# Performance work log

Hardware: AMD Instinct MI355X
Metric: run time of the kernel (lower is better)

The kernel has to match this reference:

```python
import jax, jax.numpy as jnp
import numpy as np

N = 50000
E = 800000
D_IN = 256
D_OUT = 256
EPS = 1.0 + 1e-06


def setup_inputs() -> dict:
    key = jax.random.key(0)
    ks = jax.random.split(key, 10)
    x = jax.random.normal(ks[0], (N, D_IN), dtype=jnp.float32)
    lower_indices = jax.random.randint(ks[1], (2, E), 0, N, dtype=jnp.int64)
    lower_values = jax.random.uniform(ks[2], (E,), dtype=jnp.float32)
    upper_indices = jax.random.randint(ks[3], (2, E), 0, N, dtype=jnp.int64)
    upper_values = jax.random.uniform(ks[4], (E,), dtype=jnp.float32)
    s = 1.0 / np.sqrt(D_IN)
    W_lower = jax.random.uniform(ks[5], (D_IN, D_OUT), jnp.float32, -s, s)
    att_lower = jax.random.uniform(ks[6], (2 * D_OUT,), jnp.float32, -s, s)
    W_upper = jax.random.uniform(ks[7], (D_IN, D_OUT), jnp.float32, -s, s)
    att_upper = jax.random.uniform(ks[8], (2 * D_OUT,), jnp.float32, -s, s)
    W_lin = jax.random.uniform(ks[9], (D_IN, D_OUT), jnp.float32, -s, s)
    return {"x": x, "lower_indices": lower_indices, "lower_values": lower_values,
            "upper_indices": upper_indices, "upper_values": upper_values,
            "W_lower": W_lower, "att_lower": att_lower,
            "W_upper": W_upper, "att_upper": att_upper, "W_lin": W_lin}


def can_conv(x, indices, values, W, att_weight):
    # x: [N, d_in]; indices: [2, E] (row=target i, col=source j); values: [E]
    n = x.shape[0]
    xm = x @ W                                    # [N, d_out]
    tgt, src = indices[0], indices[1]
    d = xm.shape[1]
    # attention: elu( [x_i ; x_j] . att_weight ) computed without concat
    score = jax.nn.elu(xm @ att_weight[:d])[tgt] + jax.nn.elu(0.0) * 0.0  # placeholder
    score = jax.nn.elu((xm @ att_weight[:d])[tgt] + (xm @ att_weight[d:])[src])  # [E]
    v = score * values                            # attention * neighborhood values
    # sparse row-wise softmax (per target index)
    m = jax.ops.segment_max(v, tgt, num_segments=n)
    e = jnp.exp(v - m[tgt])
    s = jax.ops.segment_sum(e, tgt, num_segments=n)
    a = e / s[tgt]                                # [E]
    # spmm: out[i] = sum_j a_ij * xm[j]
    return jax.ops.segment_sum(a[:, None] * xm[src], tgt, num_segments=n)


def reference(x, lower_indices, lower_values, upper_indices, upper_values,
              W_lower, att_lower, W_upper, att_upper, W_lin):
    lower_x = can_conv(x, lower_indices, lower_values, W_lower, att_lower)
    upper_x = can_conv(x, upper_indices, upper_values, W_upper, att_upper)
    w_x = (x @ W_lin) * EPS
    return jax.nn.relu(lower_x + upper_x + w_x)
```

## Files before the change

kernel.cpp:

```cpp
#include <hip/hip_runtime.h>
#include <hip/hip_bf16.h>


constexpr int N_NODES = 50000;
constexpr int N_EDGES = 800000;
constexpr int D = 256;
constexpr float EPSV = 1.0f + 1e-06f;

typedef __attribute__((ext_vector_type(8))) short short8;
typedef __attribute__((ext_vector_type(4))) float f32x4;

__device__ __forceinline__ unsigned short f2bf(float f) {
    unsigned int b = __float_as_uint(f);
    unsigned int r = (b + 0x7FFFu + ((b >> 16) & 1u)) >> 16;
    return (unsigned short)r;
}
__device__ __forceinline__ float bf2f(unsigned short u) {
    return __uint_as_float(((unsigned int)u) << 16);
}

__global__ __launch_bounds__(256) void cvt_x_kernel(
    const float4* __restrict__ x, ushort4* __restrict__ xb, int n4)
{
    int i = blockIdx.x * 256 + threadIdx.x;
    if (i >= n4) return;
    float4 v = x[i];
    ushort4 o;
    o.x = f2bf(v.x); o.y = f2bf(v.y); o.z = f2bf(v.z); o.w = f2bf(v.w);
    xb[i] = o;
}

__global__ __launch_bounds__(256) void cvt_w_kernel(
    const float* __restrict__ W0, const float* __restrict__ W1,
    const float* __restrict__ W2, unsigned short* __restrict__ wbT)
{
    int z = blockIdx.y;
    const float* W = (z == 0) ? W0 : (z == 1) ? W1 : W2;
    int n = blockIdx.x;
    int k = threadIdx.x;
    wbT[(size_t)z * 65536 + (size_t)n * 256 + k] = f2bf(W[(size_t)k * 256 + n]);
}

__global__ __launch_bounds__(256) void gemm_mfma_kernel(
    const unsigned short* __restrict__ xb, const unsigned short* __restrict__ wbT,
    unsigned short* __restrict__ xml, unsigned short* __restrict__ xmu,
    float* __restrict__ out, int M)
{
    const int wz = blockIdx.z;
    const int tid = threadIdx.x;
    const int w = tid >> 6, lane = tid & 63;
    const int r16 = lane & 15, g = lane >> 4;
    const int m0 = blockIdx.x * 128 + w * 32;
    const int n0 = blockIdx.y * 64;
    const unsigned short* wb = wbT + (size_t)wz * 65536;

    const int ar0 = min(m0 + r16, M - 1);
    const int ar1 = min(m0 + 16 + r16, M - 1);
    const unsigned short* pa0 = xb + (size_t)ar0 * 256 + 8 * g;
    const unsigned short* pa1 = xb + (size_t)ar1 * 256 + 8 * g;
    const unsigned short* pb  = wb + (size_t)(n0 + r16) * 256 + 8 * g;

    f32x4 acc[2][4];
    #pragma unroll
    for (int mf = 0; mf < 2; ++mf)
        #pragma unroll
        for (int nf = 0; nf < 4; ++nf)
            acc[mf][nf] = (f32x4){0.f, 0.f, 0.f, 0.f};

    #pragma unroll
    for (int kt = 0; kt < 256; kt += 32) {
        short8 a0 = *reinterpret_cast<const short8*>(pa0 + kt);
        short8 a1 = *reinterpret_cast<const short8*>(pa1 + kt);
        #pragma unroll
        for (int nf = 0; nf < 4; ++nf) {
            short8 bf = *reinterpret_cast<const short8*>(pb + (size_t)nf * 16 * 256 + kt);
            acc[0][nf] = __builtin_amdgcn_mfma_f32_16x16x32_bf16(a0, bf, acc[0][nf], 0, 0, 0);
            acc[1][nf] = __builtin_amdgcn_mfma_f32_16x16x32_bf16(a1, bf, acc[1][nf], 0, 0, 0);
        }
    }

    if (wz < 2) {
        unsigned short* dst = wz ? xmu : xml;
        #pragma unroll
        for (int mf = 0; mf < 2; ++mf)
            #pragma unroll
            for (int r = 0; r < 4; ++r) {
                int row = m0 + mf * 16 + g * 4 + r;
                if (row < M) {
                    #pragma unroll
                    for (int nf = 0; nf < 4; ++nf)
                        dst[(size_t)row * 256 + n0 + nf * 16 + r16] = f2bf(acc[mf][nf][r]);
                }
            }
    } else {
        #pragma unroll
        for (int mf = 0; mf < 2; ++mf)
            #pragma unroll
            for (int r = 0; r < 4; ++r) {
                int row = m0 + mf * 16 + g * 4 + r;
                if (row < M) {
                    #pragma unroll
                    for (int nf = 0; nf < 4; ++nf)
                        out[(size_t)row * 256 + n0 + nf * 16 + r16] = acc[mf][nf][r] * EPSV;
                }
            }
    }
}

__global__ __launch_bounds__(256) void att_kernel(
    const unsigned short* __restrict__ xm, const float* __restrict__ att,
    float* __restrict__ a, float* __restrict__ b, int n)
{
    int node = (int)((blockIdx.x * 256 + threadIdx.x) >> 6);
    int lane = threadIdx.x & 63;
    if (node >= n) return;
    ushort4 uv = *reinterpret_cast<const ushort4*>(xm + (size_t)node * 256 + lane * 4);
    float x0 = bf2f(uv.x), x1 = bf2f(uv.y), x2 = bf2f(uv.z), x3 = bf2f(uv.w);
    int o = lane * 4;
    float sa = x0 * att[o] + x1 * att[o + 1] + x2 * att[o + 2] + x3 * att[o + 3];
    float sb = x0 * att[D + o] + x1 * att[D + o + 1] + x2 * att[D + o + 2] + x3 * att[D + o + 3];
    #pragma unroll
    for (int off = 32; off; off >>= 1) {
        sa += __shfl_down(sa, off);
        sb += __shfl_down(sb, off);
    }
    if (lane == 0) { a[node] = sa; b[node] = sb; }
}

__global__ __launch_bounds__(256) void hist_kernel(
    const int* __restrict__ il, const int* __restrict__ iu,
    int* __restrict__ cl, int* __restrict__ cu)
{
    int e = blockIdx.x * 256 + threadIdx.x;
    if (e >= N_EDGES) return;
    atomicAdd(&cl[il[e]], 1);
    atomicAdd(&cu[iu[e]], 1);
}

__global__ __launch_bounds__(1024) void scan_local_kernel(
    const int* __restrict__ cnt0, int* __restrict__ ro0,
    const int* __restrict__ cnt1, int* __restrict__ ro1,
    int* __restrict__ bsum, int n)
{
    int c = blockIdx.y;
    const int* cnt = c ? cnt1 : cnt0;
    int* ro = c ? ro1 : ro0;
    __shared__ int sm[1024];
    int tid = threadIdx.x;
    int i = blockIdx.x * 1024 + tid;
    int v = (i < n) ? cnt[i] : 0;
    sm[tid] = v;
    __syncthreads();
    #pragma unroll
    for (int off = 1; off < 1024; off <<= 1) {
        int t = (tid >= off) ? sm[tid - off] : 0;
        __syncthreads();
        sm[tid] += t;
        __syncthreads();
    }
    if (i < n) ro[i] = sm[tid] - v;
    if (tid == 1023) bsum[c * 64 + blockIdx.x] = sm[1023];
}

__global__ __launch_bounds__(128) void scan_bsum_kernel(int* __restrict__ bsum, int nb)
{
    int c = threadIdx.x >> 6, lane = threadIdx.x & 63;
    int v = (lane < nb) ? bsum[c * 64 + lane] : 0;
    int orig = v;
    #pragma unroll
    for (int off = 1; off < 64; off <<= 1) {
        int t = __shfl_up(v, off);
        if (lane >= off) v += t;
    }
    if (lane < nb) bsum[c * 64 + lane] = v - orig;
}

__global__ __launch_bounds__(256) void scan_apply_kernel(
    int* __restrict__ ro0, int* __restrict__ ro1,
    const int* __restrict__ bsum, int n)
{
    int c = blockIdx.y;
    int* ro = c ? ro1 : ro0;
    int i = blockIdx.x * 256 + threadIdx.x;
    if (i < n) ro[i] += bsum[c * 64 + (i >> 10)];
    if (i == 0) ro[n] = N_EDGES;
}

__global__ __launch_bounds__(256) void scatter_kernel(
    const int* __restrict__ il, const float* __restrict__ vl,
    const int* __restrict__ rol, int* __restrict__ curl, int2* __restrict__ egl,
    const int* __restrict__ iu, const float* __restrict__ vu,
    const int* __restrict__ rou, int* __restrict__ curu, int2* __restrict__ egu)
{
    int e = blockIdx.x * 256 + threadIdx.x;
    if (e >= N_EDGES) return;
    int tl = il[e];
    int pl = rol[tl] + atomicAdd(&curl[tl], 1);
    int2 p; p.x = il[N_EDGES + e]; p.y = __float_as_int(vl[e]);
    egl[pl] = p;
    int tu = iu[e];
    int pu = rou[tu] + atomicAdd(&curu[tu], 1);
    int2 q; q.x = iu[N_EDGES + e]; q.y = __float_as_int(vu[e]);
    egu[pu] = q;
}

__device__ __forceinline__ float wave_sum(float v) {
    #pragma unroll
    for (int off = 32; off; off >>= 1) v += __shfl_xor(v, off);
    return v;
}

__device__ __forceinline__ void conv_accum(
    int node, int lane,
    const int* __restrict__ ro, const int2* __restrict__ eg,
    const float* __restrict__ a, const float* __restrict__ b,
    const unsigned short* __restrict__ xm, float4& acc)
{
    int rs = ro[node], re = ro[node + 1];
    int deg = re - rs;
    if (deg <= 0) return;
    float ai = a[node];
    if (deg <= 64) {
        float evl = 0.f; int srcl = 0;
        if (lane < deg) {
            int2 p = eg[rs + lane];
            srcl = p.x;
            float xv = ai + b[srcl];
            float sc = (xv > 0.f) ? xv : (expf(xv) - 1.f);
            evl = expf(sc * __int_as_float(p.y));
        }
        float invs = 1.f / wave_sum(evl);
        for (int t = 0; t < deg; ++t) {
            float w = __shfl(evl, t) * invs;
            int si = __shfl(srcl, t);
            ushort4 uv = *reinterpret_cast<const ushort4*>(xm + (size_t)si * 256 + lane * 4);
            acc.x += w * bf2f(uv.x); acc.y += w * bf2f(uv.y);
            acc.z += w * bf2f(uv.z); acc.w += w * bf2f(uv.w);
        }
    } else {
        float s = 0.f;
        for (int c = rs; c < re; c += 64) {
            int m = min(64, re - c);
            float evl = 0.f;
            if (lane < m) {
                int2 p = eg[c + lane];
                float xv = ai + b[p.x];
                float sc = (xv > 0.f) ? xv : (expf(xv) - 1.f);
                evl = expf(sc * __int_as_float(p.y));
            }
            s += wave_sum(evl);
        }
        float invs = 1.f / s;
        for (int c = rs; c < re; c += 64) {
            int m = min(64, re - c);
            float evl = 0.f; int srcl = 0;
            if (lane < m) {
                int2 p = eg[c + lane];
                srcl = p.x;
                float xv = ai + b[srcl];
                float sc = (xv > 0.f) ? xv : (expf(xv) - 1.f);
                evl = expf(sc * __int_as_float(p.y));
            }
            for (int t = 0; t < m; ++t) {
                float w = __shfl(evl, t) * invs;
                int si = __shfl(srcl, t);
                ushort4 uv = *reinterpret_cast<const ushort4*>(xm + (size_t)si * 256 + lane * 4);
                acc.x += w * bf2f(uv.x); acc.y += w * bf2f(uv.y);
                acc.z += w * bf2f(uv.z); acc.w += w * bf2f(uv.w);
            }
        }
    }
}

__global__ __launch_bounds__(256) void gather_kernel(
    const int* __restrict__ rol, const int2* __restrict__ egl,
    const float* __restrict__ al, const float* __restrict__ bl,
    const unsigned short* __restrict__ xml,
    const int* __restrict__ rou, const int2* __restrict__ egu,
    const float* __restrict__ au, const float* __restrict__ bu,
    const unsigned short* __restrict__ xmu,
    float4* __restrict__ out)
{
    int node = (int)((blockIdx.x * 256 + threadIdx.x) >> 6);
    int lane = threadIdx.x & 63;
    if (node >= N_NODES) return;
    float4 acc = make_float4(0.f, 0.f, 0.f, 0.f);
    conv_accum(node, lane, rol, egl, al, bl, xml, acc);
    conv_accum(node, lane, rou, egu, au, bu, xmu, acc);
    float4 xw = out[(size_t)node * 64 + lane];
    acc.x = fmaxf(acc.x + xw.x, 0.f);
    acc.y = fmaxf(acc.y + xw.y, 0.f);
    acc.z = fmaxf(acc.z + xw.z, 0.f);
    acc.w = fmaxf(acc.w + xw.w, 0.f);
    out[(size_t)node * 64 + lane] = acc;
}

extern "C" void kernel_launch(void* const* d_in, const int* in_sizes, int n_in,
                              void* d_out, int out_size, void* d_ws, size_t ws_size,
                              hipStream_t stream)
{
    (void)in_sizes; (void)n_in; (void)out_size; (void)ws_size;
    const float* x        = (const float*)d_in[0];
    const int*   low_idx  = (const int*)  d_in[1];
    const float* low_vals = (const float*)d_in[2];
    const int*   up_idx   = (const int*)  d_in[3];
    const float* up_vals  = (const float*)d_in[4];
    const float* W_lower  = (const float*)d_in[5];
    const float* att_low  = (const float*)d_in[6];
    const float* W_upper  = (const float*)d_in[7];
    const float* att_up   = (const float*)d_in[8];
    const float* W_lin    = (const float*)d_in[9];
    float* out = (float*)d_out;

    char* ws = (char*)d_ws;
    size_t off = 0;
    auto alloc = [&](size_t bytes) {
        void* p = ws + off;
        off += (bytes + 255) & ~(size_t)255;
        return p;
    };
    unsigned short* xb     = (unsigned short*)alloc((size_t)N_NODES * D * 2);
    unsigned short* wbT    = (unsigned short*)alloc((size_t)3 * 256 * 256 * 2);
    unsigned short* xm_low = (unsigned short*)alloc((size_t)N_NODES * D * 2);
    unsigned short* xm_up  = (unsigned short*)alloc((size_t)N_NODES * D * 2);
    float* a_low  = (float*)alloc(N_NODES * 4);
    float* b_low  = (float*)alloc(N_NODES * 4);
    float* a_up   = (float*)alloc(N_NODES * 4);
    float* b_up   = (float*)alloc(N_NODES * 4);
    int* zero_blk = (int*)alloc(4 * N_NODES * 4);
    int* cnt_low = zero_blk;
    int* cnt_up  = zero_blk + N_NODES;
    int* cur_low = zero_blk + 2 * N_NODES;
    int* cur_up  = zero_blk + 3 * N_NODES;
    int* ro_low  = (int*)alloc((N_NODES + 1) * 4);
    int* ro_up   = (int*)alloc((N_NODES + 1) * 4);
    int* bsum    = (int*)alloc(2 * 64 * 4);
    int2* eg_low = (int2*)alloc((size_t)N_EDGES * 8);
    int2* eg_up  = (int2*)alloc((size_t)N_EDGES * 8);

    hipMemsetAsync(zero_blk, 0, 4 * N_NODES * 4, stream);

    int n4 = N_NODES * D / 4;
    cvt_x_kernel<<<(n4 + 255) / 256, 256, 0, stream>>>(
        (const float4*)x, (ushort4*)xb, n4);
    dim3 wgrid(256, 3);
    cvt_w_kernel<<<wgrid, 256, 0, stream>>>(W_lower, W_upper, W_lin, wbT);

    dim3 ggrid((N_NODES + 127) / 128, D / 64, 3);
    gemm_mfma_kernel<<<ggrid, 256, 0, stream>>>(xb, wbT, xm_low, xm_up, out, N_NODES);

    int ablocks = (N_NODES + 3) / 4;
    att_kernel<<<ablocks, 256, 0, stream>>>(xm_low, att_low, a_low, b_low, N_NODES);
    att_kernel<<<ablocks, 256, 0, stream>>>(xm_up,  att_up,  a_up,  b_up,  N_NODES);

    int eblocks = (N_EDGES + 255) / 256;
    hist_kernel<<<eblocks, 256, 0, stream>>>(low_idx, up_idx, cnt_low, cnt_up);
    dim3 sgrid((N_NODES + 1023) / 1024, 2);
    scan_local_kernel<<<sgrid, 1024, 0, stream>>>(cnt_low, ro_low, cnt_up, ro_up,
                                                  bsum, N_NODES);
    scan_bsum_kernel<<<1, 128, 0, stream>>>(bsum, (N_NODES + 1023) / 1024);
    dim3 agrid((N_NODES + 255) / 256, 2);
    scan_apply_kernel<<<agrid, 256, 0, stream>>>(ro_low, ro_up, bsum, N_NODES);
    scatter_kernel<<<eblocks, 256, 0, stream>>>(
        low_idx, low_vals, ro_low, cur_low, eg_low,
        up_idx,  up_vals,  ro_up,  cur_up,  eg_up);

    int gblocks = (N_NODES + 3) / 4;
    gather_kernel<<<gblocks, 256, 0, stream>>>(
        ro_low, eg_low, a_low, b_low, xm_low,
        ro_up,  eg_up,  a_up,  b_up,  xm_up,
        (float4*)out);
}
```

Measured before the change: 538.3 us.

## Fuse attention projections into GEMM, record edge ranks in histogram, unroll gather

The GEMM kernel now computes all three weight products per 32-row tile in one block and reduces the attention dot products from the fp32 accumulators through shared memory, removing the two separate att_kernel passes over xm. The histogram kernel stores each edge's atomic rank so the scatter kernel no longer needs a second round of atomics or the cur arrays. The gather inner loop is unrolled by two to keep two row loads in flight. The costs are higher register pressure from 24 accumulator tiles per wave, and extra rank buffers that must be written and read back.

After: 483.5 us. 10.2% less time.

```diff
diff --git a/kernel.cpp b/kernel.cpp
--- a/kernel.cpp
+++ b/kernel.cpp
@@ -41,100 +41,128 @@
     wbT[(size_t)z * 65536 + (size_t)n * 256 + k] = f2bf(W[(size_t)k * 256 + n]);
 }
 
-__global__ __launch_bounds__(256) void gemm_mfma_kernel(
+__global__ __launch_bounds__(256) void gemm_fused_kernel(
     const unsigned short* __restrict__ xb, const unsigned short* __restrict__ wbT,
+    const float* __restrict__ att_l, const float* __restrict__ att_u,
     unsigned short* __restrict__ xml, unsigned short* __restrict__ xmu,
-    float* __restrict__ out, int M)
-{
-    const int wz = blockIdx.z;
+    float* __restrict__ out,
+    float* __restrict__ al, float* __restrict__ bl,
+    float* __restrict__ au, float* __restrict__ bu, int M)
+{
     const int tid = threadIdx.x;
     const int w = tid >> 6, lane = tid & 63;
     const int r16 = lane & 15, g = lane >> 4;
-    const int m0 = blockIdx.x * 128 + w * 32;
-    const int n0 = blockIdx.y * 64;
-    const unsigned short* wb = wbT + (size_t)wz * 65536;
+    const int m0 = blockIdx.x * 32;
+    const int n0 = w * 64;
 
     const int ar0 = min(m0 + r16, M - 1);
     const int ar1 = min(m0 + 16 + r16, M - 1);
     const unsigned short* pa0 = xb + (size_t)ar0 * 256 + 8 * g;
     const unsigned short* pa1 = xb + (size_t)ar1 * 256 + 8 * g;
-    const unsigned short* pb  = wb + (size_t)(n0 + r16) * 256 + 8 * g;
-
-    f32x4 acc[2][4];
-    #pragma unroll
-    for (int mf = 0; mf < 2; ++mf)
+    const unsigned short* pb  = wbT + (size_t)(n0 + r16) * 256 + 8 * g;
+
+    f32x4 acc[3][2][4];
+    #pragma unroll
+    for (int z = 0; z < 3; ++z)
         #pragma unroll
-        for (int nf = 0; nf < 4; ++nf)
-            acc[mf][nf] = (f32x4){0.f, 0.f, 0.f, 0.f};
+        for (int mf = 0; mf < 2; ++mf)
+            #pragma unroll
+            for (int nf = 0; nf < 4; ++nf)
+                acc[z][mf][nf] = (f32x4){0.f, 0.f, 0.f, 0.f};
 
     #pragma unroll
     for (int kt = 0; kt < 256; kt += 32) {
         short8 a0 = *reinterpret_cast<const short8*>(pa0 + kt);
         short8 a1 = *reinterpret_cast<const short8*>(pa1 + kt);
         #pragma unroll
+        for (int z = 0; z < 3; ++z) {
+            #pragma unroll
+            for (int nf = 0; nf < 4; ++nf) {
+                short8 bf = *reinterpret_cast<const short8*>(
+                    pb + (size_t)z * 65536 + (size_t)nf * 16 * 256 + kt);
+                acc[z][0][nf] = __builtin_amdgcn_mfma_f32_16x16x32_bf16(a0, bf, acc[z][0][nf], 0, 0, 0);
+                acc[z][1][nf] = __builtin_amdgcn_mfma_f32_16x16x32_bf16(a1, bf, acc[z][1][nf], 0, 0, 0);
+            }
+        }
+    }
+
+    #pragma unroll
+    for (int mf = 0; mf < 2; ++mf)
+        #pragma unroll
+        for (int r = 0; r < 4; ++r) {
+            int row = m0 + mf * 16 + g * 4 + r;
+            if (row < M) {
+                #pragma unroll
+                for (int nf = 0; nf < 4; ++nf) {
+                    int col = n0 + nf * 16 + r16;
+                    xml[(size_t)row * 256 + col] = f2bf(acc[0][mf][nf][r]);
+                    xmu[(size_t)row * 256 + col] = f2bf(acc[1][mf][nf][r]);
+                    out[(size_t)row * 256 + col] = acc[2][mf][nf][r] * EPSV;
+                }
+            }
+        }
+
+    float attv[2][2][4];
+    #pragma unroll
+    for (int h = 0; h < 2; ++h)
+        #pragma unroll
         for (int nf = 0; nf < 4; ++nf) {
-            short8 bf = *reinterpret_cast<const short8*>(pb + (size_t)nf * 16 * 256 + kt);
-            acc[0][nf] = __builtin_amdgcn_mfma_f32_16x16x32_bf16(a0, bf, acc[0][nf], 0, 0, 0);
-            acc[1][nf] = __builtin_amdgcn_mfma_f32_16x16x32_bf16(a1, bf, acc[1][nf], 0, 0, 0);
-        }
-    }
-
-    if (wz < 2) {
-        unsigned short* dst = wz ? xmu : xml;
+            int c = h * 256 + n0 + nf * 16 + r16;
+            attv[0][h][nf] = att_l[c];
+            attv[1][h][nf] = att_u[c];
+        }
+
+    __shared__ float red[4][32][4];
+    #pragma unroll
+    for (int mf = 0; mf < 2; ++mf)
         #pragma unroll
-        for (int mf = 0; mf < 2; ++mf)
+        for (int r = 0; r < 4; ++r) {
+            float p[4];
             #pragma unroll
-            for (int r = 0; r < 4; ++r) {
-                int row = m0 + mf * 16 + g * 4 + r;
-                if (row < M) {
+            for (int z = 0; z < 2; ++z)
+                #pragma unroll
+                for (int h = 0; h < 2; ++h) {
+                    float s = 0.f;
                     #pragma unroll
                     for (int nf = 0; nf < 4; ++nf)
-                        dst[(size_t)row * 256 + n0 + nf * 16 + r16] = f2bf(acc[mf][nf][r]);
+                        s += acc[z][mf][nf][r] * attv[z][h][nf];
+                    p[z * 2 + h] = s;
                 }
+            #pragma unroll
+            for (int off = 1; off < 16; off <<= 1)
+                #pragma unroll
+                for (int c = 0; c < 4; ++c)
+                    p[c] += __shfl_xor(p[c], off);
+            if (r16 == 0) {
+                int row_loc = mf * 16 + g * 4 + r;
+                red[w][row_loc][0] = p[0];
+                red[w][row_loc][1] = p[1];
+                red[w][row_loc][2] = p[2];
+                red[w][row_loc][3] = p[3];
             }
-    } else {
-        #pragma unroll
-        for (int mf = 0; mf < 2; ++mf)
-            #pragma unroll
-            for (int r = 0; r < 4; ++r) {
-                int row = m0 + mf * 16 + g * 4 + r;
-                if (row < M) {
-                    #pragma unroll
-                    for (int nf = 0; nf < 4; ++nf)
-                        out[(size_t)row * 256 + n0 + nf * 16 + r16] = acc[mf][nf][r] * EPSV;
-                }
-            }
-    }
-}
-
-__global__ __launch_bounds__(256) void att_kernel(
-    const unsigned short* __restrict__ xm, const float* __restrict__ att,
-    float* __restrict__ a, float* __restrict__ b, int n)
-{
-    int node = (int)((blockIdx.x * 256 + threadIdx.x) >> 6);
-    int lane = threadIdx.x & 63;
-    if (node >= n) return;
-    ushort4 uv = *reinterpret_cast<const ushort4*>(xm + (size_t)node * 256 + lane * 4);
-    float x0 = bf2f(uv.x), x1 = bf2f(uv.y), x2 = bf2f(uv.z), x3 = bf2f(uv.w);
-    int o = lane * 4;
-    float sa = x0 * att[o] + x1 * att[o + 1] + x2 * att[o + 2] + x3 * att[o + 3];
-    float sb = x0 * att[D + o] + x1 * att[D + o + 1] + x2 * att[D + o + 2] + x3 * att[D + o + 3];
-    #pragma unroll
-    for (int off = 32; off; off >>= 1) {
-        sa += __shfl_down(sa, off);
-        sb += __shfl_down(sb, off);
-    }
-    if (lane == 0) { a[node] = sa; b[node] = sb; }
+        }
+    __syncthreads();
+    if (tid < 128) {
+        int row_loc = tid >> 2, comp = tid & 3;
+        int row = m0 + row_loc;
+        if (row < M) {
+            float s = red[0][row_loc][comp] + red[1][row_loc][comp]
+                    + red[2][row_loc][comp] + red[3][row_loc][comp];
+            float* dst = (comp == 0) ? al : (comp == 1) ? bl : (comp == 2) ? au : bu;
+            dst[row] = s;
+        }
+    }
 }
 
 __global__ __launch_bounds__(256) void hist_kernel(
     const int* __restrict__ il, const int* __restrict__ iu,
-    int* __restrict__ cl, int* __restrict__ cu)
+    int* __restrict__ cl, int* __restrict__ cu,
+    int* __restrict__ rkl, int* __restrict__ rku)
 {
     int e = blockIdx.x * 256 + threadIdx.x;
     if (e >= N_EDGES) return;
-    atomicAdd(&cl[il[e]], 1);
-    atomicAdd(&cu[iu[e]], 1);
+    rkl[e] = atomicAdd(&cl[il[e]], 1);
+    rku[e] = atomicAdd(&cu[iu[e]], 1);
 }
 
 __global__ __launch_bounds__(1024) void scan_local_kernel(
@@ -188,26 +216,50 @@
 
 __global__ __launch_bounds__(256) void scatter_kernel(
     const int* __restrict__ il, const float* __restrict__ vl,
-    const int* __restrict__ rol, int* __restrict__ curl, int2* __restrict__ egl,
+    const int* __restrict__ rol, const int* __restrict__ rkl, int2* __restrict__ egl,
     const int* __restrict__ iu, const float* __restrict__ vu,
-    const int* __restrict__ rou, int* __restrict__ curu, int2* __restrict__ egu)
+    const int* __restrict__ rou, const int* __restrict__ rku, int2* __restrict__ egu)
 {
     int e = blockIdx.x * 256 + threadIdx.x;
     if (e >= N_EDGES) return;
-    int tl = il[e];
-    int pl = rol[tl] + atomicAdd(&curl[tl], 1);
     int2 p; p.x = il[N_EDGES + e]; p.y = __float_as_int(vl[e]);
-    egl[pl] = p;
-    int tu = iu[e];
-    int pu = rou[tu] + atomicAdd(&curu[tu], 1);
+    egl[rol[il[e]] + rkl[e]] = p;
     int2 q; q.x = iu[N_EDGES + e]; q.y = __float_as_int(vu[e]);
-    egu[pu] = q;
+    egu[rou[iu[e]] + rku[e]] = q;
 }
 
 __device__ __forceinline__ float wave_sum(float v) {
     #pragma unroll
     for (int off = 32; off; off >>= 1) v += __shfl_xor(v, off);
     return v;
+}
+
+__device__ __forceinline__ void pv_accum(
+    int lane, float invs, float evl, int srcl, int t0, int m,
+    const unsigned short* __restrict__ xm, float4& acc)
+{
+    int t = t0;
+    for (; t + 2 <= m; t += 2) {
+        float w0 = __shfl(evl, t) * invs;
+        int   s0 = __shfl(srcl, t);
+        float w1 = __shfl(evl, t + 1) * invs;
+        int   s1 = __shfl(srcl, t + 1);
+        ushort4 u0 = *reinterpret_cast<const ushort4*>(xm + (size_t)s0 * 256 + lane * 4);
+        ushort4 u1 = *reinterpret_cast<const ushort4*>(xm + (size_t)s1 * 256 + lane * 4);
+        acc.x += w0 * bf2f(u0.x) + w1 * bf2f(u1.x);
+        acc.y += w0 * bf2f(u0.y) + w1 * bf2f(u1.y);
+        acc.z += w0 * bf2f(u0.z) + w1 * bf2f(u1.z);
+        acc.w += w0 * bf2f(u0.w) + w1 * bf2f(u1.w);
+    }
+    if (t < m) {
+        float w0 = __shfl(evl, t) * invs;
+        int   s0 = __shfl(srcl, t);
+        ushort4 u0 = *reinterpret_cast<const ushort4*>(xm + (size_t)s0 * 256 + lane * 4);
+        acc.x += w0 * bf2f(u0.x);
+        acc.y += w0 * bf2f(u0.y);
+        acc.z += w0 * bf2f(u0.z);
+        acc.w += w0 * bf2f(u0.w);
+    }
 }
 
 __device__ __forceinline__ void conv_accum(
@@ -230,13 +282,7 @@
             evl = expf(sc * __int_as_float(p.y));
         }
         float invs = 1.f / wave_sum(evl);
-        for (int t = 0; t < deg; ++t) {
-            float w = __shfl(evl, t) * invs;
-            int si = __shfl(srcl, t);
-            ushort4 uv = *reinterpret_cast<const ushort4*>(xm + (size_t)si * 256 + lane * 4);
-            acc.x += w * bf2f(uv.x); acc.y += w * bf2f(uv.y);
-            acc.z += w * bf2f(uv.z); acc.w += w * bf2f(uv.w);
-        }
+        pv_accum(lane, invs, evl, srcl, 0, deg, xm, acc);
     } else {
         float s = 0.f;
         for (int c = rs; c < re; c += 64) {
@@ -261,13 +307,7 @@
                 float sc = (xv > 0.f) ? xv : (expf(xv) - 1.f);
                 evl = expf(sc * __int_as_float(p.y));
             }
-            for (int t = 0; t < m; ++t) {
-                float w = __shfl(evl, t) * invs;
-                int si = __shfl(srcl, t);
-                ushort4 uv = *reinterpret_cast<const ushort4*>(xm + (size_t)si * 256 + lane * 4);
-                acc.x += w * bf2f(uv.x); acc.y += w * bf2f(uv.y);
-                acc.z += w * bf2f(uv.z); acc.w += w * bf2f(uv.w);
-            }
+            pv_accum(lane, invs, evl, srcl, 0, m, xm, acc);
         }
     }
 }
@@ -327,18 +367,18 @@
     float* b_low  = (float*)alloc(N_NODES * 4);
     float* a_up   = (float*)alloc(N_NODES * 4);
     float* b_up   = (float*)alloc(N_NODES * 4);
-    int* zero_blk = (int*)alloc(4 * N_NODES * 4);
+    int* zero_blk = (int*)alloc(2 * N_NODES * 4);
     int* cnt_low = zero_blk;
     int* cnt_up  = zero_blk + N_NODES;
-    int* cur_low = zero_blk + 2 * N_NODES;
-    int* cur_up  = zero_blk + 3 * N_NODES;
+    int* rk_low  = (int*)alloc((size_t)N_EDGES * 4);
+    int* rk_up   = (int*)alloc((size_t)N_EDGES * 4);
     int* ro_low  = (int*)alloc((N_NODES + 1) * 4);
     int* ro_up   = (int*)alloc((N_NODES + 1) * 4);
     int* bsum    = (int*)alloc(2 * 64 * 4);
     int2* eg_low = (int2*)alloc((size_t)N_EDGES * 8);
     int2* eg_up  = (int2*)alloc((size_t)N_EDGES * 8);
 
-    hipMemsetAsync(zero_blk, 0, 4 * N_NODES * 4, stream);
+    hipMemsetAsync(zero_blk, 0, 2 * N_NODES * 4, stream);
 
     int n4 = N_NODES * D / 4;
     cvt_x_kernel<<<(n4 + 255) / 256, 256, 0, stream>>>(
@@ -346,15 +386,14 @@
     dim3 wgrid(256, 3);
     cvt_w_kernel<<<wgrid, 256, 0, stream>>>(W_lower, W_upper, W_lin, wbT);
 
-    dim3 ggrid((N_NODES + 127) / 128, D / 64, 3);
-    gemm_mfma_kernel<<<ggrid, 256, 0, stream>>>(xb, wbT, xm_low, xm_up, out, N_NODES);
-
-    int ablocks = (N_NODES + 3) / 4;
-    att_kernel<<<ablocks, 256, 0, stream>>>(xm_low, att_low, a_low, b_low, N_NODES);
-    att_kernel<<<ablocks, 256, 0, stream>>>(xm_up,  att_up,  a_up,  b_up,  N_NODES);
+    int gemmblocks = (N_NODES + 31) / 32;
+    gemm_fused_kernel<<<gemmblocks, 256, 0, stream>>>(
+        xb, wbT, att_low, att_up, xm_low, xm_up, out,
+        a_low, b_low, a_up, b_up, N_NODES);
 
     int eblocks = (N_EDGES + 255) / 256;
-    hist_kernel<<<eblocks, 256, 0, stream>>>(low_idx, up_idx, cnt_low, cnt_up);
+    hist_kernel<<<eblocks, 256, 0, stream>>>(low_idx, up_idx, cnt_low, cnt_up,
+                                             rk_low, rk_up);
     dim3 sgrid((N_NODES + 1023) / 1024, 2);
     scan_local_kernel<<<sgrid, 1024, 0, stream>>>(cnt_low, ro_low, cnt_up, ro_up,
                                                   bsum, N_NODES);
@@ -362,8 +401,8 @@
     dim3 agrid((N_NODES + 255) / 256, 2);
     scan_apply_kernel<<<agrid, 256, 0, stream>>>(ro_low, ro_up, bsum, N_NODES);
     scatter_kernel<<<eblocks, 256, 0, stream>>>(
-        low_idx, low_vals, ro_low, cur_low, eg_low,
-        up_idx,  up_vals,  ro_up,  cur_up,  eg_up);
+        low_idx, low_vals, ro_low, rk_low, eg_low,
+        up_idx,  up_vals,  ro_up,  rk_up,  eg_up);
 
     int gblocks = (N_NODES + 3) / 4;
     gather_kernel<<<gblocks, 256, 0, stream>>>(
```
